# Kernel tuning notes

Measured on AMD Instinct MI355X. Metric: run time of the kernel, lower is better.

## Reference

```python
import jax, jax.numpy as jnp
import numpy as np

NUM_LABELS = 10  # number of distinct label values in the minibatch
EPS = 1e-8


def setup_inputs() -> dict:
    key = jax.random.key(0)
    k1, k2 = jax.random.split(key)
    z = jax.random.normal(k1, (8192, 20, 256), dtype=jnp.float32)  # [B, C, H]
    labels = jax.random.randint(k2, (8192,), 0, NUM_LABELS)  # [B]
    return {"z": z, "labels": labels}


def reference(z, labels):
    # CODI minibatch loss, positive pairs, representation space.
    # Equivalent to: for each unique label, mse(z[group] + 1e-8, mean(z[group]))
    # summed over labels. Vectorized as a single segment-mean +
    # gather-broadcast + segment-SSE pass (one traversal of z).
    z = jnp.nan_to_num(z)
    B, C, H = z.shape
    counts = jax.ops.segment_sum(
        jnp.ones((B,), dtype=z.dtype), labels, num_segments=NUM_LABELS
    )  # [K]
    sums = jax.ops.segment_sum(z, labels, num_segments=NUM_LABELS)  # [K, C, H]
    means = jnp.nan_to_num(sums / jnp.maximum(counts, 1.0)[:, None, None])
    # per-sample squared distance to its group's mean (note the +EPS as in torch)
    d = (z + EPS) - means[labels]  # [B, C, H]
    per_sample = jnp.sum(d * d, axis=(1, 2))  # [B]
    sse = jax.ops.segment_sum(per_sample, labels, num_segments=NUM_LABELS)  # [K]
    # nn.MSELoss is a mean over all elements of the group: count_k * C * H
    mse_k = sse / (jnp.maximum(counts, 1.0) * (C * H))
    # torch.unique only visits labels present in the batch -> mask empty groups
    return jnp.sum(jnp.where(counts > 0, jnp.nan_to_num(mse_k), 0.0))
```

## Files before the change

### kernel.cpp

```cpp
#include <hip/hip_runtime.h>

#define B_SZ   8192
#define CH     5120
#define CH4    1280
#define K_LAB  10
#define EPS    1e-8f
#define FLTMAX 3.402823466e38f

#define RC_N   256
#define ROWS   32
#define CC_N   4
#define CCW    320
#define NT1    320
#define NPF    4
#define NFOLD  (K_LAB * CC_N)


__device__ __forceinline__ float4 sanitize(float4 v) {
    v.x = (v.x == v.x) ? fminf(fmaxf(v.x, -FLTMAX), FLTMAX) : 0.f;
    v.y = (v.y == v.y) ? fminf(fmaxf(v.y, -FLTMAX), FLTMAX) : 0.f;
    v.z = (v.z == v.z) ? fminf(fmaxf(v.z, -FLTMAX), FLTMAX) : 0.f;
    v.w = (v.w == v.w) ? fminf(fmaxf(v.w, -FLTMAX), FLTMAX) : 0.f;
    return v;
}

__global__ __launch_bounds__(NT1) void codi_pass1(
    const float4* __restrict__ z4, const int* __restrict__ labels,
    float4* __restrict__ P_sum, float* __restrict__ P_ssq,
    int* __restrict__ P_cnt, int* __restrict__ done)
{
    const int tid = threadIdx.x;
    const int rc  = blockIdx.x >> 2;
    const int cc  = blockIdx.x & 3;

    __shared__ int   lab_s[ROWS];
    __shared__ float wssq[5][K_LAB];

    if (blockIdx.x == 0 && tid == 0) *done = 0;

    if (tid < ROWS) lab_s[tid] = labels[rc * ROWS + tid];
    __syncthreads();

    float4 sum[K_LAB];
    float  ssq[K_LAB];
    #pragma unroll
    for (int k = 0; k < K_LAB; ++k) {
        sum[k] = make_float4(0.f, 0.f, 0.f, 0.f);
        ssq[k] = 0.f;
    }

    const float4* zp = z4 + (size_t)rc * ROWS * CH4 + cc * CCW + tid;

    #define LD(BUF, R0) do { \
        _Pragma("unroll") \
        for (int u = 0; u < NPF; ++u) BUF[u] = zp[(size_t)((R0) + u) * CH4]; \
    } while (0)

    #define EAT(BUF, R0) do { \
        _Pragma("unroll") \
        for (int u = 0; u < NPF; ++u) { \
            const int lab = __builtin_amdgcn_readfirstlane(lab_s[(R0) + u]); \
            float4 t = sanitize(BUF[u]); \
            float  q = fmaf(t.x, t.x, fmaf(t.y, t.y, fmaf(t.z, t.z, t.w * t.w))); \
            switch (lab) {    \
                case 0: ACC(0); break;  case 1: ACC(1); break; \
                case 2: ACC(2); break;  case 3: ACC(3); break; \
                case 4: ACC(4); break;  case 5: ACC(5); break; \
                case 6: ACC(6); break;  case 7: ACC(7); break; \
                case 8: ACC(8); break;  default: ACC(9); break; \
            } \
        } \
    } while (0)

    #define ACC(K) do { \
        sum[K].x += t.x; sum[K].y += t.y; \
        sum[K].z += t.z; sum[K].w += t.w; ssq[K] += q; } while (0)

    float4 va[NPF], vb[NPF];
    LD(va, 0);
    for (int r = 0; r < ROWS; r += 2 * NPF) {
        LD(vb, r + NPF);
        EAT(va, r);
        if (r + 2 * NPF < ROWS) LD(va, r + 2 * NPF);
        EAT(vb, r + NPF);
    }
    #undef ACC
    #undef EAT
    #undef LD

    #pragma unroll
    for (int k = 0; k < K_LAB; ++k)
        P_sum[(((size_t)(k * CC_N + cc)) * RC_N + rc) * CCW + tid] = sum[k];

    const int lane = tid & 63, wid = tid >> 6;
    #pragma unroll
    for (int k = 0; k < K_LAB; ++k) {
        float s = ssq[k];
        #pragma unroll
        for (int o = 32; o > 0; o >>= 1) s += __shfl_down(s, o, 64);
        if (lane == 0) wssq[wid][k] = s;
    }
    __syncthreads();
    if (tid < K_LAB)
        P_ssq[(rc * CC_N + cc) * K_LAB + tid] =
            wssq[0][tid] + wssq[1][tid] + wssq[2][tid] + wssq[3][tid] + wssq[4][tid];

    if (cc == 0 && tid < 64) {
        const int lab = (tid < ROWS) ? lab_s[tid] : -1;
        #pragma unroll
        for (int k = 0; k < K_LAB; ++k) {
            unsigned long long m = __ballot(lab == k);
            if (tid == k) P_cnt[rc * K_LAB + k] = __popcll(m);
        }
    }
}

__global__ __launch_bounds__(NT1) void codi_pass2(
    const float4* __restrict__ P_sum, const float* __restrict__ P_ssq,
    const int* __restrict__ P_cnt, float* __restrict__ pn,
    float* __restrict__ ssqk, float* __restrict__ cntk,
    int* __restrict__ done, float* __restrict__ out)
{
    const int tid  = threadIdx.x;
    const int lane = tid & 63, wid = tid >> 6;
    const int fid  = blockIdx.x;
    const int fk   = fid >> 2, fcc = fid & 3;

    __shared__ float red_q[5], red_s[5];
    __shared__ int   red_n[5];
    __shared__ int   tkt;

    const float4* p = P_sum + ((size_t)(fk * CC_N + fcc) * RC_N) * CCW + tid;
    float4 s4 = make_float4(0.f, 0.f, 0.f, 0.f);
    #pragma unroll 8
    for (int rc = 0; rc < RC_N; ++rc) {
        float4 v = p[(size_t)rc * CCW];
        s4.x += v.x; s4.y += v.y; s4.z += v.z; s4.w += v.w;
    }
    float q = fmaf(s4.x, s4.x, fmaf(s4.y, s4.y, fmaf(s4.z, s4.z, s4.w * s4.w)));
    #pragma unroll
    for (int o = 32; o > 0; o >>= 1) q += __shfl_down(q, o, 64);

    float s2 = 0.f;
    int   n  = 0;
    if (fcc == 0) {
        for (int i = tid; i < RC_N * CC_N; i += NT1) s2 += P_ssq[i * K_LAB + fk];
        if (tid < RC_N) n = P_cnt[tid * K_LAB + fk];
    }
    #pragma unroll
    for (int o = 32; o > 0; o >>= 1) s2 += __shfl_down(s2, o, 64);
    #pragma unroll
    for (int o = 32; o > 0; o >>= 1) n += __shfl_down(n, o, 64);

    if (lane == 0) { red_q[wid] = q; red_s[wid] = s2; red_n[wid] = n; }
    __syncthreads();
    if (tid == 0) {
        pn[fid] = red_q[0] + red_q[1] + red_q[2] + red_q[3] + red_q[4];
        if (fcc == 0) {
            ssqk[fk] = red_s[0] + red_s[1] + red_s[2] + red_s[3] + red_s[4];
            cntk[fk] = (float)(red_n[0] + red_n[1] + red_n[2] + red_n[3] + red_n[4]);
        }
    }

    __threadfence();
    __syncthreads();
    if (tid == 0) tkt = atomicAdd(done, 1);
    __syncthreads();
    if (tkt == NFOLD - 1 && tid < 64) {
        float np4 = (tid < NFOLD) ? atomicAdd(&pn[tid], 0.f) : 0.f;
        np4 += __shfl_down(np4, 2, 64);
        np4 += __shfl_down(np4, 1, 64);
        float s2v = (tid < K_LAB) ? atomicAdd(&ssqk[tid], 0.f) : 0.f;
        float nnv = (tid < K_LAB) ? atomicAdd(&cntk[tid], 0.f) : 0.f;
        float acc = 0.f;
        for (int k = 0; k < K_LAB; ++k) {
            float np = __shfl(np4, 4 * k, 64);
            float sk = __shfl(s2v, k, 64);
            float nk = __shfl(nnv, k, 64);
            if (nk > 0.f) {
                float sse = sk - np / nk + nk * (float)CH * (EPS * EPS);
                float mse = sse / (nk * (float)CH);
                if (mse == mse) acc += mse;
            }
        }
        if (tid == 0) out[0] = acc;
    }
}

extern "C" void kernel_launch(void* const* d_in, const int* in_sizes, int n_in,
                              void* d_out, int out_size, void* d_ws, size_t ws_size,
                              hipStream_t stream) {
    const float4* z4     = (const float4*)d_in[0];
    const int*    labels = (const int*)d_in[1];

    float*  hdr   = (float*)d_ws;
    int*    done  = (int*)hdr;
    float*  pn    = hdr + 16;
    float*  ssqk  = hdr + 64;
    float*  cntk  = hdr + 80;
    int*    P_cnt = (int*)(hdr + 96);
    float*  P_ssq = hdr + 2688;
    float4* P_sum = (float4*)(hdr + 13056);

    codi_pass1<<<RC_N * CC_N, NT1, 0, stream>>>(z4, labels, P_sum, P_ssq, P_cnt, done);
    codi_pass2<<<NFOLD, NT1, 0, stream>>>(P_sum, P_ssq, P_cnt, pn, ssqk,
                                          cntk, done, (float*)d_out);
}
```

Measured before the change: 287.2 us.

## Sort rows by label in-block and accumulate one running group sum

Pass 1 now builds a per-block permutation of its 32 rows grouped by label, using ballot and popcount, and loads rows in that order. Instead of keeping ten float4 accumulators selected by a switch, it keeps a single running sum and flushes it to P_sum and shared memory whenever the label group changes. This is meant to cut register pressure and the per-row branch, raising occupancy on the memory-bound pass. In exchange, loads become gathers through an LDS index, and the flush loop adds wave reductions and a data-dependent while loop in the inner code.

```diff
diff --git a/kernel.cpp b/kernel.cpp
--- a/kernel.cpp
+++ b/kernel.cpp
@@ -29,90 +29,88 @@
     float4* __restrict__ P_sum, float* __restrict__ P_ssq,
     int* __restrict__ P_cnt, int* __restrict__ done)
 {
-    const int tid = threadIdx.x;
-    const int rc  = blockIdx.x >> 2;
-    const int cc  = blockIdx.x & 3;
-
-    __shared__ int   lab_s[ROWS];
+    const int tid  = threadIdx.x;
+    const int lane = tid & 63, wid = tid >> 6;
+    const int rc   = blockIdx.x >> 2;
+    const int cc   = blockIdx.x & 3;
+
+    __shared__ int   perm_s[ROWS];
+    __shared__ int   starts_s[K_LAB + 1];
     __shared__ float wssq[5][K_LAB];
 
     if (blockIdx.x == 0 && tid == 0) *done = 0;
-
-    if (tid < ROWS) lab_s[tid] = labels[rc * ROWS + tid];
-    __syncthreads();
-
-    float4 sum[K_LAB];
-    float  ssq[K_LAB];
-    #pragma unroll
-    for (int k = 0; k < K_LAB; ++k) {
-        sum[k] = make_float4(0.f, 0.f, 0.f, 0.f);
-        ssq[k] = 0.f;
-    }
-
-    const float4* zp = z4 + (size_t)rc * ROWS * CH4 + cc * CCW + tid;
-
-    #define LD(BUF, R0) do { \
+    if (tid < 5 * K_LAB) ((float*)wssq)[tid] = 0.f;
+
+    if (tid < 64) {
+        const int lab = (tid < ROWS) ? labels[rc * ROWS + tid] : -1;
+        const unsigned long long ltm = (1ULL << lane) - 1ULL;
+        int base = 0;
+        #pragma unroll
+        for (int k = 0; k < K_LAB; ++k) {
+            unsigned long long m = __ballot(lab == k);
+            int cnt = __popcll(m);
+            if (tid == k) {
+                starts_s[k] = base;
+                if (cc == 0) P_cnt[rc * K_LAB + k] = cnt;
+            }
+            if (lab == k) perm_s[base + __popcll(m & ltm)] = tid;
+            base += cnt;
+        }
+        if (tid == 0) starts_s[K_LAB] = ROWS;
+    }
+    __syncthreads();
+
+    const float4* zp  = z4 + (size_t)rc * ROWS * CH4 + cc * CCW + tid;
+    float4*       psb = P_sum + ((size_t)cc * RC_N + rc) * CCW + tid;
+
+    float4 cs = make_float4(0.f, 0.f, 0.f, 0.f);
+    float  cq = 0.f;
+    int    kcur = 0;
+    int    nb   = starts_s[1];
+
+    #define FLUSH() do { \
+        psb[(size_t)kcur * (CC_N * RC_N * CCW)] = cs; \
+        float qq = cq; \
         _Pragma("unroll") \
-        for (int u = 0; u < NPF; ++u) BUF[u] = zp[(size_t)((R0) + u) * CH4]; \
+        for (int o = 32; o > 0; o >>= 1) qq += __shfl_down(qq, o, 64); \
+        if (lane == 0) wssq[wid][kcur] += qq; \
+        cs = make_float4(0.f, 0.f, 0.f, 0.f); cq = 0.f; \
     } while (0)
 
-    #define EAT(BUF, R0) do { \
+    #define LDP(BUF, I0) do { \
+        _Pragma("unroll") \
+        for (int u = 0; u < NPF; ++u) \
+            BUF[u] = zp[(size_t)perm_s[(I0) + u] * CH4]; \
+    } while (0)
+
+    #define CONS(BUF, I0) do { \
         _Pragma("unroll") \
         for (int u = 0; u < NPF; ++u) { \
-            const int lab = __builtin_amdgcn_readfirstlane(lab_s[(R0) + u]); \
+            while ((I0) + u >= nb) {           \
+                FLUSH(); ++kcur; nb = starts_s[kcur + 1]; \
+            } \
             float4 t = sanitize(BUF[u]); \
             float  q = fmaf(t.x, t.x, fmaf(t.y, t.y, fmaf(t.z, t.z, t.w * t.w))); \
-            switch (lab) {    \
-                case 0: ACC(0); break;  case 1: ACC(1); break; \
-                case 2: ACC(2); break;  case 3: ACC(3); break; \
-                case 4: ACC(4); break;  case 5: ACC(5); break; \
-                case 6: ACC(6); break;  case 7: ACC(7); break; \
-                case 8: ACC(8); break;  default: ACC(9); break; \
-            } \
-        } \
-    } while (0)
-
-    #define ACC(K) do { \
-        sum[K].x += t.x; sum[K].y += t.y; \
-        sum[K].z += t.z; sum[K].w += t.w; ssq[K] += q; } while (0)
+            cs.x += t.x; cs.y += t.y; cs.z += t.z; cs.w += t.w; cq += q; \
+        } } while (0)
 
     float4 va[NPF], vb[NPF];
-    LD(va, 0);
-    for (int r = 0; r < ROWS; r += 2 * NPF) {
-        LD(vb, r + NPF);
-        EAT(va, r);
-        if (r + 2 * NPF < ROWS) LD(va, r + 2 * NPF);
-        EAT(vb, r + NPF);
-    }
-    #undef ACC
-    #undef EAT
-    #undef LD
-
-    #pragma unroll
-    for (int k = 0; k < K_LAB; ++k)
-        P_sum[(((size_t)(k * CC_N + cc)) * RC_N + rc) * CCW + tid] = sum[k];
-
-    const int lane = tid & 63, wid = tid >> 6;
-    #pragma unroll
-    for (int k = 0; k < K_LAB; ++k) {
-        float s = ssq[k];
-        #pragma unroll
-        for (int o = 32; o > 0; o >>= 1) s += __shfl_down(s, o, 64);
-        if (lane == 0) wssq[wid][k] = s;
-    }
+    LDP(va, 0);
+    for (int i = 0; i < ROWS; i += 2 * NPF) {
+        LDP(vb, i + NPF);
+        CONS(va, i);
+        if (i + 2 * NPF < ROWS) LDP(va, i + 2 * NPF);
+        CONS(vb, i + NPF);
+    }
+    for (; kcur < K_LAB; ++kcur) FLUSH();
+    #undef CONS
+    #undef LDP
+    #undef FLUSH
+
     __syncthreads();
     if (tid < K_LAB)
         P_ssq[(rc * CC_N + cc) * K_LAB + tid] =
             wssq[0][tid] + wssq[1][tid] + wssq[2][tid] + wssq[3][tid] + wssq[4][tid];
-
-    if (cc == 0 && tid < 64) {
-        const int lab = (tid < ROWS) ? lab_s[tid] : -1;
-        #pragma unroll
-        for (int k = 0; k < K_LAB; ++k) {
-            unsigned long long m = __ballot(lab == k);
-            if (tid == k) P_cnt[rc * K_LAB + k] = __popcll(m);
-        }
-    }
 }
 
 __global__ __launch_bounds__(NT1) void codi_pass2(
```

New measurement: 267.5 us. 1.07x faster.
